# Performance work log

Measured on AMD Instinct MI355X. Metric: run time of the kernel, lower is better.

The kernel has to match this reference:

```python
import jax, jax.numpy as jnp
from jax import lax
import numpy as np

N, L, LQ, D, AF, K = 4096, 512, 32, 30, 10, 4  # n_sents, sent_len, q_len, embed_dim, extra feats, conv size


def setup_inputs() -> dict:
    key = jax.random.key(0)
    ks = jax.random.split(key, 10)
    fan_conv = 1.0 / np.sqrt(D * K)
    fan_lin = 1.0 / np.sqrt(AF + 3)
    return {
        "sents_embeds": jax.random.normal(ks[0], (N, L, D), jnp.float32),
        "question_embeds": jax.random.normal(ks[1], (LQ, D), jnp.float32),
        "sents_gaf": jax.random.normal(ks[2], (N, AF), jnp.float32),
        "sents_labels": jax.random.randint(ks[3], (N,), 0, 2),
        "conv1_w": jax.random.uniform(ks[4], (D, D, K), jnp.float32, -fan_conv, fan_conv),
        "conv1_b": jax.random.uniform(ks[5], (D,), jnp.float32, -fan_conv, fan_conv),
        "conv2_w": jax.random.uniform(ks[6], (D, D, K), jnp.float32, -fan_conv, fan_conv),
        "conv2_b": jax.random.uniform(ks[7], (D,), jnp.float32, -fan_conv, fan_conv),
        "lin_w": jax.random.uniform(ks[8], (2, AF + 3), jnp.float32, -fan_lin, fan_lin),
        "lin_b": jax.random.uniform(ks[9], (2,), jnp.float32, -fan_lin, fan_lin),
    }


def _conv1d(x, w, b):
    # x: [B, C, T], w: [O, I, K] (torch layout), padding = K-1 both sides (as torch padding=K-1)
    y = lax.conv_general_dilated(x, w, window_strides=(1,), padding=[(K - 1, K - 1)],
                                 dimension_numbers=("NCW", "OIW", "NCW"))
    return y + b[None, :, None]


def _window_pool(x):
    # avg_pool1d(kernel=K, stride=1) over last axis
    return lax.reduce_window(x, 0.0, lax.add, (1, 1, K), (1, 1, 1), "VALID") / K


def _gpool(x):
    # global average pool over last axis -> [B, C]
    return jnp.mean(x, axis=-1)


def _cos(a, b):
    # a: [N, D] or [D], b: [N, D] or [D] -> cosine similarity, broadcasting
    num = jnp.sum(a * b, axis=-1)
    den = jnp.linalg.norm(a, axis=-1) * jnp.linalg.norm(b, axis=-1)
    return num / den


def _forward(sents_embeds, question_embeds, sents_gaf, sents_labels,
             conv1_w, conv1_b, conv2_w, conv2_b, lin_w, lin_b):
    q = question_embeds.T[None]                # [1, D, LQ]
    s = jnp.transpose(sents_embeds, (0, 2, 1))  # [N, D, L]

    # question side (identical every loop iteration in the original)
    q_raw = _gpool(q)[0]                        # [D]
    q1c = _conv1d(q, conv1_w, conv1_b)          # [1, D, LQ+3]
    q1g = _gpool(q1c)[0]                        # [D]
    q1w = _window_pool(q1c)                     # [1, D, LQ]
    q2c = _conv1d(q1w, conv2_w, conv2_b)        # [1, D, LQ+3]
    q2g = _gpool(q2c)[0]                        # [D]

    # sentence side, batched over N
    s_raw = _gpool(s)                           # [N, D]
    s1c = _conv1d(s, conv1_w, conv1_b)          # [N, D, L+3]
    s1g = _gpool(s1c)                           # [N, D]
    s1w = _window_pool(s1c)                     # [N, D, L]
    s2c = _conv1d(s1w, conv2_w, conv2_b)        # [N, D, L+3]
    s2g = _gpool(s2c)                           # [N, D]

    # sim1: original overwrites quest_global_pool in the loop, so i=0 uses the raw
    # question pool and i>0 use the conv2-level question pool from the prior iter.
    sim1_raw = _cos(q_raw[None], s_raw)         # [N]
    sim1_q2 = _cos(q2g[None], s_raw)            # [N]
    sim1 = jnp.where(jnp.arange(s_raw.shape[0]) == 0, sim1_raw, sim1_q2)
    sim2 = _cos(q1g[None], s1g)                 # [N]
    sim3 = _cos(q2g[None], s2g)                 # [N]

    mlp_in = jnp.concatenate([sim1[:, None], sim2[:, None], sim3[:, None], sents_gaf], axis=-1)  # [N, 13]
    logits = mlp_in @ lin_w.T + lin_b           # [N, 2]
    logp = jax.nn.log_softmax(logits, axis=-1)
    cost = -jnp.mean(jnp.take_along_axis(logp, sents_labels[:, None], axis=-1)[:, 0])
    emit = jax.nn.softmax(logp, axis=-1)[:, 1]  # softmax applied to log_softmax, as in original
    return cost, emit


def reference(sents_embeds, question_embeds, sents_gaf, sents_labels,
              conv1_w, conv1_b, conv2_w, conv2_b, lin_w, lin_b):
    return _forward(sents_embeds, question_embeds, sents_gaf, sents_labels,
                    conv1_w, conv1_b, conv2_w, conv2_b, lin_w, lin_b)
```

## Files before the change

kernel.cpp:

```cpp
#include <hip/hip_runtime.h>
#include <math.h>

#define NS 4096
#define LL 512
#define LQS 32
#define DD 30
#define AFN 10
#define KW 4

enum {
  QRAW = 0,
  Q1G  = 30,
  Q2G  = 60,
  NRM  = 90,
  WS1  = 96,
  WS2  = 996,
  OA0  = 1896,
  OA1  = 2796,
  OA2  = 3696,
  OB0  = 4596,
  OB1  = 5496,
  OB2  = 6396,
  SARR = 7296,
  WS_TOTAL = SARR + NS * DD
};

__global__ __launch_bounds__(256) void prep_stream_kernel(
    const float* __restrict__ se,
    const float* __restrict__ qe,
    const float* __restrict__ w1,
    const float* __restrict__ b1,
    const float* __restrict__ w2,
    const float* __restrict__ b2,
    float* __restrict__ ws,
    float* __restrict__ out)
{
    const int tid = threadIdx.x;

    if (blockIdx.x != 0) {
        const int n = blockIdx.x - 1;
        const float* base = se + (size_t)n * (LL * DD);
        __shared__ float partial[960];

        if (tid < 240) {
            const float4* p = (const float4*)base + tid;
            float sx = 0.f, sy = 0.f, sz = 0.f, sw = 0.f;
            #pragma unroll
            for (int it = 0; it < 16; it++) {
                float4 v = p[it * 240];
                sx += v.x; sy += v.y; sz += v.z; sw += v.w;
            }
            partial[4 * tid + 0] = sx;
            partial[4 * tid + 1] = sy;
            partial[4 * tid + 2] = sz;
            partial[4 * tid + 3] = sw;
        }
        __syncthreads();
        if (tid < DD) {
            float a = 0.f;
            #pragma unroll
            for (int m = 0; m < 32; m++) a += partial[tid + DD * m];
            ws[SARR + n * DD + tid] = a;
        }
        return;
    }

    __shared__ float qT[DD][LQS];
    __shared__ float q1c[DD][LQS + 3];
    __shared__ float q1w[DD][LQS];
    __shared__ float q2c[DD][LQS + 3];
    __shared__ float qpool[3][DD];

    for (int f = tid; f < LQS * DD; f += 256) {
        qT[f % DD][f / DD] = qe[f];
    }
    __syncthreads();

    for (int idx = tid; idx < DD * (LQS + 3); idx += 256) {
        int o = idx / (LQS + 3), t = idx % (LQS + 3);
        float acc = b1[o];
        for (int i = 0; i < DD; i++) {
            const float* w = w1 + (o * DD + i) * KW;
            #pragma unroll
            for (int k = 0; k < KW; k++) {
                int j = t + k - 3;
                if (j >= 0 && j < LQS) acc += qT[i][j] * w[k];
            }
        }
        q1c[o][t] = acc;
    }
    __syncthreads();

    for (int idx = tid; idx < DD * LQS; idx += 256) {
        int o = idx / LQS, t = idx % LQS;
        q1w[o][t] = 0.25f * (q1c[o][t] + q1c[o][t + 1] + q1c[o][t + 2] + q1c[o][t + 3]);
    }
    __syncthreads();

    for (int idx = tid; idx < DD * (LQS + 3); idx += 256) {
        int o = idx / (LQS + 3), t = idx % (LQS + 3);
        float acc = b2[o];
        for (int i = 0; i < DD; i++) {
            const float* w = w2 + (o * DD + i) * KW;
            #pragma unroll
            for (int k = 0; k < KW; k++) {
                int j = t + k - 3;
                if (j >= 0 && j < LQS) acc += q1w[i][j] * w[k];
            }
        }
        q2c[o][t] = acc;
    }
    __syncthreads();

    if (tid < DD) {
        float a = 0.f;
        for (int t = 0; t < LQS; t++) a += qT[tid][t];
        qpool[0][tid] = a * (1.0f / LQS);
        float g1 = 0.f;
        for (int t = 0; t < LQS + 3; t++) g1 += q1c[tid][t];
        qpool[1][tid] = g1 * (1.0f / (LQS + 3));
        float g2 = 0.f;
        for (int t = 0; t < LQS + 3; t++) g2 += q2c[tid][t];
        qpool[2][tid] = g2 * (1.0f / (LQS + 3));
        ws[QRAW + tid] = qpool[0][tid];
        ws[Q1G + tid]  = qpool[1][tid];
        ws[Q2G + tid]  = qpool[2][tid];
    }
    __syncthreads();
    if (tid < 3) {
        float s = 0.f;
        for (int i = 0; i < DD; i++) { float v = qpool[tid][i]; s += v * v; }
        ws[NRM + tid] = sqrtf(s);
    }
    if (tid == 0) out[0] = 0.0f;

    for (int idx = tid; idx < DD * DD; idx += 256) {
        int o = idx / DD, i = idx % DD;
        int tr = i * DD + o;
        const float* w = w1 + idx * KW;
        float a = w[0], b = w[1], c = w[2], d = w[3];
        ws[WS1 + tr] = a + b + c + d;
        ws[OA0 + tr] = 3.f * d + 2.f * c + b;
        ws[OA1 + tr] = 2.f * d + c;
        ws[OA2 + tr] = d;
        ws[OB0 + tr] = a;
        ws[OB1 + tr] = b + 2.f * a;
        ws[OB2 + tr] = c + 2.f * b + 3.f * a;
        const float* v = w2 + idx * KW;
        ws[WS2 + tr] = v[0] + v[1] + v[2] + v[3];
    }
}

__global__ __launch_bounds__(256) void post_kernel(
    const float* __restrict__ se,
    const float* __restrict__ gaf,
    const int*   __restrict__ labels,
    const float* __restrict__ b1,
    const float* __restrict__ b2,
    const float* __restrict__ linw,
    const float* __restrict__ linb,
    const float* __restrict__ ws,
    float* __restrict__ out)
{
    const int tid  = threadIdx.x;
    const int wid  = tid >> 6;
    const int lane = tid & 63;
    const int n    = blockIdx.x * 4 + wid;

    __shared__ float costp[4];

    const bool act = (lane < DD);
    const int  ic  = act ? lane : 0;

    float S_i, e0r, e1r, e2r, e3r, e4r, e5r, bb1, bb2;
    {
        const float* base = se + (size_t)n * (LL * DD);
        S_i = ws[SARR + n * DD + ic];
        e0r = base[0 * DD + ic];
        e1r = base[1 * DD + ic];
        e2r = base[2 * DD + ic];
        e3r = base[509 * DD + ic];
        e4r = base[510 * DD + ic];
        e5r = base[511 * DD + ic];
        bb1 = b1[ic];
        bb2 = b2[ic];
    }

    float dotS = 0.f, edge = 0.f;
    #pragma unroll 6
    for (int ii = 0; ii < DD; ii++) {
        float s   = __shfl(S_i, ii, 64);
        float b0  = __shfl(e0r, ii, 64);
        float b1v = __shfl(e1r, ii, 64);
        float b2v = __shfl(e2r, ii, 64);
        float b3v = __shfl(e3r, ii, 64);
        float b4v = __shfl(e4r, ii, 64);
        float b5v = __shfl(e5r, ii, 64);
        const int t = ii * DD + ic;
        dotS += s * ws[WS1 + t];
        edge += b0 * ws[OA0 + t] + b1v * ws[OA1 + t] + b2v * ws[OA2 + t]
              + b3v * ws[OB0 + t] + b4v * ws[OB1 + t] + b5v * ws[OB2 + t];
    }
    float s1g = dotS * (1.0f / (LL + 3)) + bb1;
    float Tv  = dotS + (float)LL * bb1 - 0.25f * edge;

    float dot2 = 0.f;
    #pragma unroll 6
    for (int ii = 0; ii < DD; ii++) {
        float tv = __shfl(Tv, ii, 64);
        dot2 += tv * ws[WS2 + ii * DD + ic];
    }
    float s2g = dot2 * (1.0f / (LL + 3)) + bb2;

    float qv = (n == 0) ? ws[QRAW + ic] : ws[Q2G + ic];
    float q1 = ws[Q1G + ic];
    float q2 = ws[Q2G + ic];
    float p0 = act ? qv * S_i : 0.f;
    float p1 = act ? S_i * S_i : 0.f;
    float p2 = act ? q1 * s1g : 0.f;
    float p3 = act ? s1g * s1g : 0.f;
    float p4 = act ? q2 * s2g : 0.f;
    float p5 = act ? s2g * s2g : 0.f;
    #pragma unroll
    for (int off = 32; off >= 1; off >>= 1) {
        p0 += __shfl_xor(p0, off, 64);
        p1 += __shfl_xor(p1, off, 64);
        p2 += __shfl_xor(p2, off, 64);
        p3 += __shfl_xor(p3, off, 64);
        p4 += __shfl_xor(p4, off, 64);
        p5 += __shfl_xor(p5, off, 64);
    }

    if (lane == 0) {
        float nq = (n == 0) ? ws[NRM + 0] : ws[NRM + 2];
        float sim1 = p0 / (nq * sqrtf(p1));
        float sim2 = p2 / (ws[NRM + 1] * sqrtf(p3));
        float sim3 = p4 / (ws[NRM + 2] * sqrtf(p5));

        float in[3 + AFN];
        in[0] = sim1; in[1] = sim2; in[2] = sim3;
        const float* g = gaf + (size_t)n * AFN;
        #pragma unroll
        for (int j = 0; j < AFN; j++) in[3 + j] = g[j];

        float l0 = linb[0], l1 = linb[1];
        #pragma unroll
        for (int j = 0; j < 3 + AFN; j++) {
            l0 += in[j] * linw[j];
            l1 += in[j] * linw[(3 + AFN) + j];
        }
        float m = fmaxf(l0, l1);
        float lse = m + logf(expf(l0 - m) + expf(l1 - m));
        float lp0 = l0 - lse, lp1 = l1 - lse;
        float mm = fmaxf(lp0, lp1);
        float ee0 = expf(lp0 - mm), ee1 = expf(lp1 - mm);
        out[1 + n] = ee1 / (ee0 + ee1);
        int lab = labels[n];
        float lp = (lab == 0) ? lp0 : lp1;
        costp[wid] = -lp * (1.0f / NS);
    }
    __syncthreads();
    if (tid == 0) {
        atomicAdd(&out[0], costp[0] + costp[1] + costp[2] + costp[3]);
    }
}

extern "C" void kernel_launch(void* const* d_in, const int* in_sizes, int n_in,
                              void* d_out, int out_size, void* d_ws, size_t ws_size,
                              hipStream_t stream)
{
    (void)in_sizes; (void)n_in; (void)out_size; (void)ws_size;
    const float* se  = (const float*)d_in[0];
    const float* qe  = (const float*)d_in[1];
    const float* gaf = (const float*)d_in[2];
    const int*   lab = (const int*)d_in[3];
    const float* w1  = (const float*)d_in[4];
    const float* b1  = (const float*)d_in[5];
    const float* w2  = (const float*)d_in[6];
    const float* b2  = (const float*)d_in[7];
    const float* lw  = (const float*)d_in[8];
    const float* lb  = (const float*)d_in[9];
    float* out = (float*)d_out;
    float* ws  = (float*)d_ws;

    hipLaunchKernelGGL(prep_stream_kernel, dim3(NS + 1), dim3(256), 0, stream,
                       se, qe, w1, b1, w2, b2, ws, out);
    hipLaunchKernelGGL(post_kernel, dim3(NS / 4), dim3(256), 0, stream,
                       se, gaf, lab, b1, b2, lw, lb, ws, out);
}
```

Measured before the change: 472.3 us.

## Fuse per-sentence streaming reduction into the post kernel and stage weights in LDS

The per-sentence column-sum reduction moves out of the big prep kernel and into the post kernel, which now runs one block per sentence, so the sums no longer round-trip through the workspace. The prep kernel shrinks to a single block that first copies the conv weights into shared memory. Each post block copies the weight tables (about 29 KB) into LDS and loads the boundary rows cooperatively. In exchange, the large single-block prep now runs serially ahead of the streaming work instead of overlapping it, and every block makes its own atomicAdd to the cost.

```diff
diff --git a/kernel.cpp b/kernel.cpp
--- a/kernel.cpp
+++ b/kernel.cpp
@@ -21,12 +21,10 @@
   OB0  = 4596,
   OB1  = 5496,
   OB2  = 6396,
-  SARR = 7296,
-  WS_TOTAL = SARR + NS * DD
+  WTOT = 7296
 };
 
-__global__ __launch_bounds__(256) void prep_stream_kernel(
-    const float* __restrict__ se,
+__global__ __launch_bounds__(256) void prep_kernel(
     const float* __restrict__ qe,
     const float* __restrict__ w1,
     const float* __restrict__ b1,
@@ -35,42 +33,19 @@
     float* __restrict__ ws,
     float* __restrict__ out)
 {
-    const int tid = threadIdx.x;
-
-    if (blockIdx.x != 0) {
-        const int n = blockIdx.x - 1;
-        const float* base = se + (size_t)n * (LL * DD);
-        __shared__ float partial[960];
-
-        if (tid < 240) {
-            const float4* p = (const float4*)base + tid;
-            float sx = 0.f, sy = 0.f, sz = 0.f, sw = 0.f;
-            #pragma unroll
-            for (int it = 0; it < 16; it++) {
-                float4 v = p[it * 240];
-                sx += v.x; sy += v.y; sz += v.z; sw += v.w;
-            }
-            partial[4 * tid + 0] = sx;
-            partial[4 * tid + 1] = sy;
-            partial[4 * tid + 2] = sz;
-            partial[4 * tid + 3] = sw;
-        }
-        __syncthreads();
-        if (tid < DD) {
-            float a = 0.f;
-            #pragma unroll
-            for (int m = 0; m < 32; m++) a += partial[tid + DD * m];
-            ws[SARR + n * DD + tid] = a;
-        }
-        return;
-    }
-
+    __shared__ float w1s[DD * DD * KW];
+    __shared__ float w2s[DD * DD * KW];
     __shared__ float qT[DD][LQS];
     __shared__ float q1c[DD][LQS + 3];
     __shared__ float q1w[DD][LQS];
     __shared__ float q2c[DD][LQS + 3];
     __shared__ float qpool[3][DD];
-
+    const int tid = threadIdx.x;
+
+    for (int f = tid; f < DD * DD * KW; f += 256) {
+        w1s[f] = w1[f];
+        w2s[f] = w2[f];
+    }
     for (int f = tid; f < LQS * DD; f += 256) {
         qT[f % DD][f / DD] = qe[f];
     }
@@ -80,7 +55,7 @@
         int o = idx / (LQS + 3), t = idx % (LQS + 3);
         float acc = b1[o];
         for (int i = 0; i < DD; i++) {
-            const float* w = w1 + (o * DD + i) * KW;
+            const float* w = w1s + (o * DD + i) * KW;
             #pragma unroll
             for (int k = 0; k < KW; k++) {
                 int j = t + k - 3;
@@ -101,7 +76,7 @@
         int o = idx / (LQS + 3), t = idx % (LQS + 3);
         float acc = b2[o];
         for (int i = 0; i < DD; i++) {
-            const float* w = w2 + (o * DD + i) * KW;
+            const float* w = w2s + (o * DD + i) * KW;
             #pragma unroll
             for (int k = 0; k < KW; k++) {
                 int j = t + k - 3;
@@ -132,12 +107,13 @@
         for (int i = 0; i < DD; i++) { float v = qpool[tid][i]; s += v * v; }
         ws[NRM + tid] = sqrtf(s);
     }
+    if (tid >= 3 && tid < 6) ws[NRM + tid] = 0.f;
     if (tid == 0) out[0] = 0.0f;
 
     for (int idx = tid; idx < DD * DD; idx += 256) {
         int o = idx / DD, i = idx % DD;
         int tr = i * DD + o;
-        const float* w = w1 + idx * KW;
+        const float* w = w1s + idx * KW;
         float a = w[0], b = w[1], c = w[2], d = w[3];
         ws[WS1 + tr] = a + b + c + d;
         ws[OA0 + tr] = 3.f * d + 2.f * c + b;
@@ -146,12 +122,12 @@
         ws[OB0 + tr] = a;
         ws[OB1 + tr] = b + 2.f * a;
         ws[OB2 + tr] = c + 2.f * b + 3.f * a;
-        const float* v = w2 + idx * KW;
+        const float* v = w2s + idx * KW;
         ws[WS2 + tr] = v[0] + v[1] + v[2] + v[3];
     }
 }
 
-__global__ __launch_bounds__(256) void post_kernel(
+__global__ __launch_bounds__(256) void stream_post_kernel(
     const float* __restrict__ se,
     const float* __restrict__ gaf,
     const int*   __restrict__ labels,
@@ -162,106 +138,126 @@
     const float* __restrict__ ws,
     float* __restrict__ out)
 {
-    const int tid  = threadIdx.x;
-    const int wid  = tid >> 6;
-    const int lane = tid & 63;
-    const int n    = blockIdx.x * 4 + wid;
-
-    __shared__ float costp[4];
-
-    const bool act = (lane < DD);
-    const int  ic  = act ? lane : 0;
-
-    float S_i, e0r, e1r, e2r, e3r, e4r, e5r, bb1, bb2;
+    const int n   = blockIdx.x;
+    const int tid = threadIdx.x;
+    const float* base = se + (size_t)n * (LL * DD);
+
+    __shared__ float tabs[WTOT];
+    __shared__ float partial[960];
+    __shared__ float bnd[6][DD];
+
     {
-        const float* base = se + (size_t)n * (LL * DD);
-        S_i = ws[SARR + n * DD + ic];
-        e0r = base[0 * DD + ic];
-        e1r = base[1 * DD + ic];
-        e2r = base[2 * DD + ic];
-        e3r = base[509 * DD + ic];
-        e4r = base[510 * DD + ic];
-        e5r = base[511 * DD + ic];
-        bb1 = b1[ic];
-        bb2 = b2[ic];
-    }
-
-    float dotS = 0.f, edge = 0.f;
-    #pragma unroll 6
-    for (int ii = 0; ii < DD; ii++) {
-        float s   = __shfl(S_i, ii, 64);
-        float b0  = __shfl(e0r, ii, 64);
-        float b1v = __shfl(e1r, ii, 64);
-        float b2v = __shfl(e2r, ii, 64);
-        float b3v = __shfl(e3r, ii, 64);
-        float b4v = __shfl(e4r, ii, 64);
-        float b5v = __shfl(e5r, ii, 64);
-        const int t = ii * DD + ic;
-        dotS += s * ws[WS1 + t];
-        edge += b0 * ws[OA0 + t] + b1v * ws[OA1 + t] + b2v * ws[OA2 + t]
-              + b3v * ws[OB0 + t] + b4v * ws[OB1 + t] + b5v * ws[OB2 + t];
-    }
-    float s1g = dotS * (1.0f / (LL + 3)) + bb1;
-    float Tv  = dotS + (float)LL * bb1 - 0.25f * edge;
-
-    float dot2 = 0.f;
-    #pragma unroll 6
-    for (int ii = 0; ii < DD; ii++) {
-        float tv = __shfl(Tv, ii, 64);
-        dot2 += tv * ws[WS2 + ii * DD + ic];
-    }
-    float s2g = dot2 * (1.0f / (LL + 3)) + bb2;
-
-    float qv = (n == 0) ? ws[QRAW + ic] : ws[Q2G + ic];
-    float q1 = ws[Q1G + ic];
-    float q2 = ws[Q2G + ic];
-    float p0 = act ? qv * S_i : 0.f;
-    float p1 = act ? S_i * S_i : 0.f;
-    float p2 = act ? q1 * s1g : 0.f;
-    float p3 = act ? s1g * s1g : 0.f;
-    float p4 = act ? q2 * s2g : 0.f;
-    float p5 = act ? s2g * s2g : 0.f;
-    #pragma unroll
-    for (int off = 32; off >= 1; off >>= 1) {
-        p0 += __shfl_xor(p0, off, 64);
-        p1 += __shfl_xor(p1, off, 64);
-        p2 += __shfl_xor(p2, off, 64);
-        p3 += __shfl_xor(p3, off, 64);
-        p4 += __shfl_xor(p4, off, 64);
-        p5 += __shfl_xor(p5, off, 64);
-    }
-
-    if (lane == 0) {
-        float nq = (n == 0) ? ws[NRM + 0] : ws[NRM + 2];
-        float sim1 = p0 / (nq * sqrtf(p1));
-        float sim2 = p2 / (ws[NRM + 1] * sqrtf(p3));
-        float sim3 = p4 / (ws[NRM + 2] * sqrtf(p5));
-
-        float in[3 + AFN];
-        in[0] = sim1; in[1] = sim2; in[2] = sim3;
-        const float* g = gaf + (size_t)n * AFN;
-        #pragma unroll
-        for (int j = 0; j < AFN; j++) in[3 + j] = g[j];
-
-        float l0 = linb[0], l1 = linb[1];
-        #pragma unroll
-        for (int j = 0; j < 3 + AFN; j++) {
-            l0 += in[j] * linw[j];
-            l1 += in[j] * linw[(3 + AFN) + j];
-        }
-        float m = fmaxf(l0, l1);
-        float lse = m + logf(expf(l0 - m) + expf(l1 - m));
-        float lp0 = l0 - lse, lp1 = l1 - lse;
-        float mm = fmaxf(lp0, lp1);
-        float ee0 = expf(lp0 - mm), ee1 = expf(lp1 - mm);
-        out[1 + n] = ee1 / (ee0 + ee1);
-        int lab = labels[n];
-        float lp = (lab == 0) ? lp0 : lp1;
-        costp[wid] = -lp * (1.0f / NS);
-    }
-    __syncthreads();
-    if (tid == 0) {
-        atomicAdd(&out[0], costp[0] + costp[1] + costp[2] + costp[3]);
+        const float4* src = (const float4*)ws;
+        float4* dst = (float4*)tabs;
+        #pragma unroll
+        for (int f = tid; f < WTOT / 4; f += 256) dst[f] = src[f];
+    }
+    if (tid < 240) {
+        const float4* p = (const float4*)base + tid;
+        float sx = 0.f, sy = 0.f, sz = 0.f, sw = 0.f;
+        #pragma unroll
+        for (int it = 0; it < 16; it++) {
+            float4 v = p[it * 240];
+            sx += v.x; sy += v.y; sz += v.z; sw += v.w;
+        }
+        partial[4 * tid + 0] = sx;
+        partial[4 * tid + 1] = sy;
+        partial[4 * tid + 2] = sz;
+        partial[4 * tid + 3] = sw;
+    }
+    if (tid < 180) {
+        int r = tid / DD, c = tid % DD;
+        int j = (r < 3) ? r : (LL - 6 + r);
+        bnd[r][c] = base[j * DD + c];
+    }
+    __syncthreads();
+
+    if (tid < 64) {
+        const int lane = tid;
+        const bool act = (lane < DD);
+        const int  ic  = act ? lane : 0;
+
+        float S_i = 0.f;
+        #pragma unroll
+        for (int m = 0; m < 32; m++) S_i += partial[ic + DD * m];
+
+        float e0r = bnd[0][ic], e1r = bnd[1][ic], e2r = bnd[2][ic];
+        float e3r = bnd[3][ic], e4r = bnd[4][ic], e5r = bnd[5][ic];
+        float bb1 = b1[ic], bb2 = b2[ic];
+
+        float dotS = 0.f, edge = 0.f;
+        #pragma unroll 6
+        for (int ii = 0; ii < DD; ii++) {
+            float s   = __shfl(S_i, ii, 64);
+            float b0  = __shfl(e0r, ii, 64);
+            float b1v = __shfl(e1r, ii, 64);
+            float b2v = __shfl(e2r, ii, 64);
+            float b3v = __shfl(e3r, ii, 64);
+            float b4v = __shfl(e4r, ii, 64);
+            float b5v = __shfl(e5r, ii, 64);
+            const int t = ii * DD + ic;
+            dotS += s * tabs[WS1 + t];
+            edge += b0 * tabs[OA0 + t] + b1v * tabs[OA1 + t] + b2v * tabs[OA2 + t]
+                  + b3v * tabs[OB0 + t] + b4v * tabs[OB1 + t] + b5v * tabs[OB2 + t];
+        }
+        float s1g = dotS * (1.0f / (LL + 3)) + bb1;
+        float Tv  = dotS + (float)LL * bb1 - 0.25f * edge;
+
+        float dot2 = 0.f;
+        #pragma unroll 6
+        for (int ii = 0; ii < DD; ii++) {
+            float tv = __shfl(Tv, ii, 64);
+            dot2 += tv * tabs[WS2 + ii * DD + ic];
+        }
+        float s2g = dot2 * (1.0f / (LL + 3)) + bb2;
+
+        float qv = (n == 0) ? tabs[QRAW + ic] : tabs[Q2G + ic];
+        float q1 = tabs[Q1G + ic];
+        float q2 = tabs[Q2G + ic];
+        float p0 = act ? qv * S_i : 0.f;
+        float p1 = act ? S_i * S_i : 0.f;
+        float p2 = act ? q1 * s1g : 0.f;
+        float p3 = act ? s1g * s1g : 0.f;
+        float p4 = act ? q2 * s2g : 0.f;
+        float p5 = act ? s2g * s2g : 0.f;
+        #pragma unroll
+        for (int off = 32; off >= 1; off >>= 1) {
+            p0 += __shfl_xor(p0, off, 64);
+            p1 += __shfl_xor(p1, off, 64);
+            p2 += __shfl_xor(p2, off, 64);
+            p3 += __shfl_xor(p3, off, 64);
+            p4 += __shfl_xor(p4, off, 64);
+            p5 += __shfl_xor(p5, off, 64);
+        }
+
+        if (lane == 0) {
+            float nq = (n == 0) ? tabs[NRM + 0] : tabs[NRM + 2];
+            float sim1 = p0 / (nq * sqrtf(p1));
+            float sim2 = p2 / (tabs[NRM + 1] * sqrtf(p3));
+            float sim3 = p4 / (tabs[NRM + 2] * sqrtf(p5));
+
+            float in[3 + AFN];
+            in[0] = sim1; in[1] = sim2; in[2] = sim3;
+            const float* g = gaf + (size_t)n * AFN;
+            #pragma unroll
+            for (int j = 0; j < AFN; j++) in[3 + j] = g[j];
+
+            float l0 = linb[0], l1 = linb[1];
+            #pragma unroll
+            for (int j = 0; j < 3 + AFN; j++) {
+                l0 += in[j] * linw[j];
+                l1 += in[j] * linw[(3 + AFN) + j];
+            }
+            float m = fmaxf(l0, l1);
+            float lse = m + logf(expf(l0 - m) + expf(l1 - m));
+            float lp0 = l0 - lse, lp1 = l1 - lse;
+            float mm = fmaxf(lp0, lp1);
+            float ee0 = expf(lp0 - mm), ee1 = expf(lp1 - mm);
+            out[1 + n] = ee1 / (ee0 + ee1);
+            int lab = labels[n];
+            float lp = (lab == 0) ? lp0 : lp1;
+            atomicAdd(&out[0], -lp * (1.0f / NS));
+        }
     }
 }
 
@@ -283,8 +279,8 @@
     float* out = (float*)d_out;
     float* ws  = (float*)d_ws;
 
-    hipLaunchKernelGGL(prep_stream_kernel, dim3(NS + 1), dim3(256), 0, stream,
-                       se, qe, w1, b1, w2, b2, ws, out);
-    hipLaunchKernelGGL(post_kernel, dim3(NS / 4), dim3(256), 0, stream,
+    hipLaunchKernelGGL(prep_kernel, dim3(1), dim3(256), 0, stream,
+                       qe, w1, b1, w2, b2, ws, out);
+    hipLaunchKernelGGL(stream_post_kernel, dim3(NS), dim3(256), 0, stream,
                        se, gaf, lab, b1, b2, lw, lb, ws, out);
 }
```

Result: faster. 424.4 us (-10.2%).
